# Optimization experiments

Hardware: AMD Instinct MI355X
Metric: run time of the kernel (lower is better)

## Reference

```python
import jax, jax.numpy as jnp
import numpy as np

L = 6        # flow_layers
DIM = 40     # state_dim = 4*levels
H = 128      # hidden_dim
ADIM = DIM // 2
DIN = ADIM + 2 * H  # x_a + ctx + t_e (cond_dim=0)
CLIP = 2.0   # flow_scale_clip
B = 131072


def _perm_mask_indices():
    # Matches ConditionalRealNVP.__init__(seed=0): per-layer permutation uses
    # default_rng(seed+i); masks drawn sequentially from default_rng(seed).
    rng = np.random.default_rng(0)
    perms, idx_a, idx_b = [], [], []
    for i in range(L):
        perms.append(np.random.default_rng(0 + i).permutation(DIM).astype(np.int32))
        mask = np.zeros(DIM, dtype=bool)
        mask[rng.choice(DIM, size=DIM // 2, replace=False)] = True
        idx_a.append(np.nonzero(mask)[0].astype(np.int32))
        idx_b.append(np.nonzero(~mask)[0].astype(np.int32))
    return (jnp.asarray(np.stack(perms)), jnp.asarray(np.stack(idx_a)),
            jnp.asarray(np.stack(idx_b)))


def setup_inputs() -> dict:
    key = jax.random.key(0)
    ks = jax.random.split(key, 16)

    def lin(k, shape, fan_in):
        bound = 1.0 / np.sqrt(fan_in)
        return jax.random.uniform(k, shape, jnp.float32, -bound, bound)

    x = jax.random.normal(ks[0], (B, DIM), jnp.float32)
    ctx = jax.random.normal(ks[1], (B, H), jnp.float32)
    t_e = jax.random.normal(ks[2], (B, H), jnp.float32)

    W1 = lin(ks[3], (L, DIN, H), DIN); b1 = lin(ks[4], (L, H), DIN)
    W2 = lin(ks[5], (L, H, H), H);     b2 = lin(ks[6], (L, H), H)
    W3 = lin(ks[7], (L, H, H), H);     b3 = lin(ks[8], (L, H), H)
    Ws = lin(ks[9], (L, H, ADIM), H);  bs = lin(ks[10], (L, ADIM), H)
    Wt = lin(ks[11], (L, H, ADIM), H); bt = lin(ks[12], (L, ADIM), H)

    perm, idx_a, idx_b = _perm_mask_indices()
    return dict(x=x, ctx=ctx, t_e=t_e, W1=W1, b1=b1, W2=W2, b2=b2, W3=W3, b3=b3,
                Ws=Ws, bs=bs, Wt=Wt, bt=bt, perm=perm, idx_a=idx_a, idx_b=idx_b)


def reference(x, ctx, t_e, W1, b1, W2, b2, W3, b3, Ws, bs, Wt, bt, perm, idx_a, idx_b):
    # ConditionalRealNVP.forward: per layer -> permute, mask-split, backbone MLP,
    # clamped affine scale/shift on x_b, scatter-merge, accumulate logdet.
    z = x
    logdet = jnp.zeros(x.shape[0], dtype=x.dtype)
    for i in range(L):
        z = z[:, perm[i]]                      # invertible permutation [B, DIM]
        z_a = z[:, idx_a[i]]                   # [B, ADIM] masked gather
        z_b = z[:, idx_b[i]]                   # [B, ADIM]
        h = jnp.concatenate([z_a, ctx, t_e], axis=-1)  # [B, DIN]
        h = jax.nn.silu(h @ W1[i] + b1[i])
        h = jax.nn.silu(h @ W2[i] + b2[i])
        h = jax.nn.silu(h @ W3[i] + b3[i])     # [B, H]
        s = jnp.clip(h @ Ws[i] + bs[i], -CLIP, CLIP)
        t = h @ Wt[i] + bt[i]
        y_b = z_b * jnp.exp(s) + t
        z = jnp.zeros_like(z).at[:, idx_a[i]].set(z_a).at[:, idx_b[i]].set(y_b)
        logdet = logdet + s.sum(axis=-1)
    return z, logdet
```

## Files before the change

kernel.cpp:

```cpp
#include <hip/hip_runtime.h>
#include <hip/hip_bf16.h>
#include <stdint.h>
#include <stddef.h>

typedef __bf16 bf16_t;
typedef __bf16 bf16x8 __attribute__((ext_vector_type(8)));
typedef __bf16 bf16x4 __attribute__((ext_vector_type(4)));
typedef float  f32x4  __attribute__((ext_vector_type(4)));

#define MFMA16(a, b, c) __builtin_amdgcn_mfma_f32_16x16x32_bf16((a), (b), (c), 0, 0, 0)

__device__ __forceinline__ float silu_f(float v) {
    return v * __builtin_amdgcn_rcpf(1.f + __expf(-v));
}

namespace cfg {
constexpr int B    = 131072;
constexpr int DIM  = 40;
constexpr int H    = 128;
constexpr int AD   = 20;
constexpr int L    = 6;
constexpr int MB   = 64;
constexpr int NTH  = 256;
constexpr int ZS   = 41;

constexpr int TILE  = 128 * 32;
constexpr int LTILE = 128 * 40;
constexpr int LSTR  = 21 * TILE;
constexpr int WTOT  = 6 * LSTR;
constexpr int NPH   = 6 * 21;

constexpr int CTE_BLKS = B / 16;
constexpr int W_BLKS   = WTOT / 256;
}

__device__ __align__(16) bf16_t g_wsb[cfg::WTOT];
__device__ int    g_gtab[352];
__device__ __align__(16) bf16_t g_cte[(size_t)cfg::B * 256];

__device__ __forceinline__ int woff(int an, int s) {
    return an * 40 + (((s ^ (an >> 1) ^ (an >> 3)) & 3) << 3);
}

__global__ void prep_all(const float* __restrict__ ctx, const float* __restrict__ te,
                         const float* __restrict__ W1, const float* __restrict__ W2,
                         const float* __restrict__ W3, const float* __restrict__ Ws,
                         const float* __restrict__ Wt, const int* __restrict__ perm,
                         const int* __restrict__ ia, const int* __restrict__ ib)
{
    using namespace cfg;
    __shared__ int phys_s[40], tmp_s[40], pas[20], pbs[20];
    __shared__ bf16_t cb[16 * 264];

    if (blockIdx.x < CTE_BLKS) {
        int g16 = blockIdx.x;
        int t = threadIdx.x;
        #pragma unroll
        for (int k = 0; k < 4; ++k) {
            int f4 = k * 256 + t;
            int r = f4 >> 6, c4 = (f4 & 63) * 4;
            const float* src = (c4 < 128) ? &ctx[((size_t)g16 * 16 + r) * 128 + c4]
                                          : &te[((size_t)g16 * 16 + r) * 128 + (c4 - 128)];
            float4 v = *(const float4*)src;
            bf16x4 bv;
            bv[0] = (bf16_t)v.x; bv[1] = (bf16_t)v.y; bv[2] = (bf16_t)v.z; bv[3] = (bf16_t)v.w;
            *(bf16x4*)&cb[r * 264 + c4] = bv;
        }
        __syncthreads();
        #pragma unroll
        for (int kk = 0; kk < 2; ++kk) {
            int t2 = kk * 256 + t;
            int kt = t2 >> 6, ln = t2 & 63, q = ln >> 4, c = ln & 15;
            bf16x8 o = *(const bf16x8*)&cb[c * 264 + kt * 32 + q * 8];
            *(bf16x8*)&g_cte[(size_t)g16 * 4096 + (size_t)t2 * 8] = o;
        }
        return;
    }

    int bb = blockIdx.x - CTE_BLKS;
    int t  = bb * 256 + threadIdx.x;
    {
        int i = t / LSTR, r = t % LSTR;
        int tile = r / TILE, r2 = r % TILE;
        int n = r2 >> 5, kl = r2 & 31;
        float v = 0.f;
        if (tile < 9) {
            int k = tile * 32 + kl;
            if (k < 20)       v = W1[(i * 276 + k) * 128 + n];
            else if (k >= 32) v = W1[(i * 276 + (k - 12)) * 128 + n];
        } else if (tile < 13) {
            int k = (tile - 9) * 32 + kl;
            v = W2[(i * 128 + k) * 128 + n];
        } else if (tile < 17) {
            int k = (tile - 13) * 32 + kl;
            v = W3[(i * 128 + k) * 128 + n];
        } else {
            int k = (tile - 17) * 32 + kl;
            if (n < 20)                 v = Ws[(i * 128 + k) * 20 + n];
            else if (n >= 32 && n < 52) v = Wt[(i * 128 + k) * 20 + (n - 32)];
        }
        g_wsb[t] = (bf16_t)v;
    }

    if (bb == 0) {
        int u = threadIdx.x;
        if (u < 40) phys_s[u] = u;
        __syncthreads();
        for (int i = 0; i < L; ++i) {
            if (u < 20) {
                int sa = phys_s[perm[i * 40 + ia[i * 20 + u]]];
                int sb = phys_s[perm[i * 40 + ib[i * 20 + u]]];
                pas[u] = sa; pbs[u] = sb;
                g_gtab[i * 32 + u]        = sa;
                g_gtab[192 + i * 20 + u]  = sb;
            } else if (u < 32) {
                g_gtab[i * 32 + u] = 0;
            }
            __syncthreads();
            if (u < 20) {
                tmp_s[ia[i * 20 + u]] = pas[u];
                tmp_s[ib[i * 20 + u]] = pbs[u];
            }
            __syncthreads();
            if (u < 40) phys_s[u] = tmp_s[u];
            __syncthreads();
        }
        if (u < 40) g_gtab[312 + u] = phys_s[u];
    }
}

__global__ __launch_bounds__(256, 3) void flow_main(
    const float* __restrict__ x,
    const float* __restrict__ gb1, const float* __restrict__ gb2, const float* __restrict__ gb3,
    const float* __restrict__ gbs, const float* __restrict__ gbt,
    float* __restrict__ out)
{
    using namespace cfg;
    __shared__ __align__(16) char smem[49792];
    float*  z_s  = (float*)(smem);
    bf16_t* h    = (bf16_t*)(smem + 10496);
    bf16_t* wb   = (bf16_t*)(smem + 27904);
    int*    gtab = (int*)(smem + 48384);

    const int tid  = threadIdx.x;
    const int lane = tid & 63;
    const int w    = tid >> 6;
    const int q    = lane >> 4, c = lane & 15;
    const int rw   = w * 16;
    const int cb   = w * 32 + 2 * c;
    const int row0 = blockIdx.x * MB;

    for (int e = tid; e < 352; e += NTH) gtab[e] = g_gtab[e];
    for (int e = tid; e < MB * DIM; e += NTH) {
        int r = e / DIM, d = e - r * DIM;
        z_s[r * ZS + d] = x[(size_t)row0 * DIM + e];
    }

    uint4 sg0, sg1;
    const int an0 = tid >> 2, sl0 = tid & 3;
    auto SLOAD = [&](int T) {
        const bf16_t* s = g_wsb + (size_t)T * TILE;
        sg0 = *(const uint4*)(s + tid * 8);
        sg1 = *(const uint4*)(s + 2048 + tid * 8);
    };
    auto SWRITE = [&](bf16_t* wbc) {
        *(uint4*)&wbc[woff(an0, sl0)]      = sg0;
        *(uint4*)&wbc[woff(an0 + 64, sl0)] = sg1;
    };

    SLOAD(0);
    SWRITE(wb);
    float ld[4] = {0.f, 0.f, 0.f, 0.f};
    __syncthreads();
    int cur = 0;

    for (int i = 0; i < L; ++i) {
        const int* pa = gtab + i * 32;
        const int* pb = gtab + 192 + i * 20;
        const int  T0 = i * 21;

        {
            f32x4 acc[4][2] = {};
            bf16x8 aN[4];
            #pragma unroll
            for (int kt = 0; kt < 9; ++kt) {
                bf16_t* wbc = wb + cur * LTILE;
                SLOAD(T0 + kt + 1);
                bf16x8 aK[4];
                if (kt == 0) {
                    #pragma unroll
                    for (int rf = 0; rf < 4; ++rf) {
                        bf16x8 t;
                        #pragma unroll
                        for (int j = 0; j < 8; ++j)
                            t[j] = (bf16_t)z_s[(rf * 16 + c) * ZS + pa[q * 8 + j]];
                        aK[rf] = t;
                    }
                    #pragma unroll
                    for (int rf = 0; rf < 4; ++rf)
                        aN[rf] = *(const bf16x8*)&g_cte[((size_t)(blockIdx.x * 4 + rf)) * 4096 + lane * 8];
                } else {
                    #pragma unroll
                    for (int rf = 0; rf < 4; ++rf) aK[rf] = aN[rf];
                    if (kt < 8) {
                        #pragma unroll
                        for (int rf = 0; rf < 4; ++rf)
                            aN[rf] = *(const bf16x8*)&g_cte[((size_t)(blockIdx.x * 4 + rf)) * 4096 + (size_t)kt * 512 + lane * 8];
                    }
                }
                bf16x8 b0 = *(const bf16x8*)&wbc[woff(cb, q)];
                bf16x8 b1 = *(const bf16x8*)&wbc[woff(cb + 1, q)];
                __builtin_amdgcn_s_setprio(1);
                #pragma unroll
                for (int rf = 0; rf < 4; ++rf) {
                    acc[rf][0] = MFMA16(aK[rf], b0, acc[rf][0]);
                    acc[rf][1] = MFMA16(aK[rf], b1, acc[rf][1]);
                }
                __builtin_amdgcn_s_setprio(0);
                if (kt == 8) {
                    float bv0 = gb1[i * H + cb], bv1 = gb1[i * H + cb + 1];
                    #pragma unroll
                    for (int rf = 0; rf < 4; ++rf)
                        #pragma unroll
                        for (int rr = 0; rr < 4; ++rr) {
                            float v0 = silu_f(acc[rf][0][rr] + bv0);
                            float v1 = silu_f(acc[rf][1][rr] + bv1);
                            union { bf16_t h2[2]; uint32_t u; } pk;
                            pk.h2[0] = (bf16_t)v0; pk.h2[1] = (bf16_t)v1;
                            *(uint32_t*)&h[(rf * 16 + q * 4 + rr) * 136 + cb] = pk.u;
                        }
                }
                SWRITE(wb + (cur ^ 1) * LTILE);
                __syncthreads();
                cur ^= 1;
            }
        }

        #pragma unroll
        for (int mm = 0; mm < 2; ++mm) {
            bf16x8 ah[16];
            #pragma unroll
            for (int kt = 0; kt < 4; ++kt)
                #pragma unroll
                for (int rf = 0; rf < 4; ++rf)
                    ah[kt * 4 + rf] = *(const bf16x8*)&h[(rf * 16 + c) * 136 + kt * 32 + q * 8];
            f32x4 acc[4][2] = {};
            const float* bias = (mm == 0 ? gb2 : gb3) + i * H;
            #pragma unroll
            for (int kt = 0; kt < 4; ++kt) {
                bf16_t* wbc = wb + cur * LTILE;
                SLOAD(T0 + 9 + mm * 4 + kt + 1);
                bf16x8 b0 = *(const bf16x8*)&wbc[woff(cb, q)];
                bf16x8 b1 = *(const bf16x8*)&wbc[woff(cb + 1, q)];
                __builtin_amdgcn_s_setprio(1);
                #pragma unroll
                for (int rf = 0; rf < 4; ++rf) {
                    acc[rf][0] = MFMA16(ah[kt * 4 + rf], b0, acc[rf][0]);
                    acc[rf][1] = MFMA16(ah[kt * 4 + rf], b1, acc[rf][1]);
                }
                __builtin_amdgcn_s_setprio(0);
                if (kt == 3) {
                    float bv0 = bias[cb], bv1 = bias[cb + 1];
                    #pragma unroll
                    for (int rf = 0; rf < 4; ++rf)
                        #pragma unroll
                        for (int rr = 0; rr < 4; ++rr) {
                            float v0 = silu_f(acc[rf][0][rr] + bv0);
                            float v1 = silu_f(acc[rf][1][rr] + bv1);
                            union { bf16_t h2[2]; uint32_t u; } pk;
                            pk.h2[0] = (bf16_t)v0; pk.h2[1] = (bf16_t)v1;
                            *(uint32_t*)&h[(rf * 16 + q * 4 + rr) * 136 + cb] = pk.u;
                        }
                }
                SWRITE(wb + (cur ^ 1) * LTILE);
                __syncthreads();
                cur ^= 1;
            }
        }

        {
            f32x4 sacc[4] = {};
            #pragma unroll
            for (int kt = 0; kt < 4; ++kt) {
                bf16_t* wbc = wb + cur * LTILE;
                int Tn = T0 + 18 + kt;
                if (Tn < NPH) SLOAD(Tn);
                bf16x8 af = *(const bf16x8*)&h[(rw + c) * 136 + kt * 32 + q * 8];
                __builtin_amdgcn_s_setprio(1);
                #pragma unroll
                for (int nt = 0; nt < 4; ++nt) {
                    bf16x8 bfr = *(const bf16x8*)&wbc[woff(nt * 16 + c, q)];
                    sacc[nt] = MFMA16(af, bfr, sacc[nt]);
                }
                __builtin_amdgcn_s_setprio(0);
                if (kt == 3) {
                    float bs0 = gbs[i * AD + c];
                    float bt0 = gbt[i * AD + c];
                    int   sl1 = pb[c];
                    float bs1 = 0.f, bt1 = 0.f; int sl2 = 0;
                    if (c < 4) { bs1 = gbs[i * AD + 16 + c]; bt1 = gbt[i * AD + 16 + c]; sl2 = pb[16 + c]; }
                    #pragma unroll
                    for (int rr = 0; rr < 4; ++rr) {
                        int row = rw + q * 4 + rr;
                        float s1 = fminf(fmaxf(sacc[0][rr] + bs0, -2.f), 2.f);
                        float y1 = z_s[row * ZS + sl1] * __expf(s1) + (sacc[2][rr] + bt0);
                        z_s[row * ZS + sl1] = y1;
                        float ssum = s1;
                        if (c < 4) {
                            float s2 = fminf(fmaxf(sacc[1][rr] + bs1, -2.f), 2.f);
                            float y2 = z_s[row * ZS + sl2] * __expf(s2) + (sacc[3][rr] + bt1);
                            z_s[row * ZS + sl2] = y2;
                            ssum += s2;
                        }
                        ssum += __shfl_xor(ssum, 1);
                        ssum += __shfl_xor(ssum, 2);
                        ssum += __shfl_xor(ssum, 4);
                        ssum += __shfl_xor(ssum, 8);
                        ld[rr] += ssum;
                    }
                }
                if (Tn < NPH) SWRITE(wb + (cur ^ 1) * LTILE);
                __syncthreads();
                cur ^= 1;
            }
        }
    }

    const int* fo = gtab + 312;
    for (int e = tid; e < MB * DIM; e += NTH) {
        int r = e / DIM, d = e - r * DIM;
        out[(size_t)row0 * DIM + e] = z_s[r * ZS + fo[d]];
    }
    if (c == 0) {
        #pragma unroll
        for (int rr = 0; rr < 4; ++rr)
            out[(size_t)B * DIM + row0 + rw + q * 4 + rr] = ld[rr];
    }
}

extern "C" void kernel_launch(void* const* d_in, const int* in_sizes, int n_in,
                              void* d_out, int out_size, void* d_ws, size_t ws_size,
                              hipStream_t stream) {
    using namespace cfg;
    const float* x   = (const float*)d_in[0];
    const float* ctx = (const float*)d_in[1];
    const float* te  = (const float*)d_in[2];
    const float* W1  = (const float*)d_in[3];
    const float* b1  = (const float*)d_in[4];
    const float* W2  = (const float*)d_in[5];
    const float* b2  = (const float*)d_in[6];
    const float* W3  = (const float*)d_in[7];
    const float* b3  = (const float*)d_in[8];
    const float* Ws_ = (const float*)d_in[9];
    const float* bs_ = (const float*)d_in[10];
    const float* Wt_ = (const float*)d_in[11];
    const float* bt_ = (const float*)d_in[12];
    const int* perm  = (const int*)d_in[13];
    const int* ia    = (const int*)d_in[14];
    const int* ib    = (const int*)d_in[15];

    float* out = (float*)d_out;

    prep_all<<<CTE_BLKS + W_BLKS, 256, 0, stream>>>(ctx, te, W1, W2, W3, Ws_, Wt_, perm, ia, ib);
    flow_main<<<B / MB, NTH, 0, stream>>>(x, b1, b2, b3, bs_, bt_, out);
}
```

Baseline: 482.7 us.

## Prefetch weight tiles two phases ahead with split-register staging and lighter barriers

Weight tile staging moves from one register set to two (A/B), so each global load is issued two phases before its LDS write rather than one, giving more time to hide global latency. The __syncthreads is replaced by a barrier that waits only on LDS/scalar counters (lgkmcnt), so outstanding global loads are not drained at each phase. The LDS weight row stride grows from 40 to 48 with a simpler XOR swizzle, which raises shared memory per block and adds staging registers, possibly hurting occupancy at 3 blocks/CU. The pipeline now restarts at each layer boundary, adding a prologue per layer.

```diff
diff --git a/kernel.cpp b/kernel.cpp
--- a/kernel.cpp
+++ b/kernel.cpp
@@ -13,6 +13,12 @@
 __device__ __forceinline__ float silu_f(float v) {
     return v * __builtin_amdgcn_rcpf(1.f + __expf(-v));
 }
+
+#define PHASE_BAR() do {                                   \
+    asm volatile("s_waitcnt lgkmcnt(0)" ::: "memory");     \
+    __builtin_amdgcn_s_barrier();                          \
+    __builtin_amdgcn_sched_barrier(0);                     \
+} while (0)
 
 namespace cfg {
 constexpr int B    = 131072;
@@ -25,10 +31,9 @@
 constexpr int ZS   = 41;
 
 constexpr int TILE  = 128 * 32;
-constexpr int LTILE = 128 * 40;
+constexpr int LTILE = 128 * 48;
 constexpr int LSTR  = 21 * TILE;
 constexpr int WTOT  = 6 * LSTR;
-constexpr int NPH   = 6 * 21;
 
 constexpr int CTE_BLKS = B / 16;
 constexpr int W_BLKS   = WTOT / 256;
@@ -39,7 +44,7 @@
 __device__ __align__(16) bf16_t g_cte[(size_t)cfg::B * 256];
 
 __device__ __forceinline__ int woff(int an, int s) {
-    return an * 40 + (((s ^ (an >> 1) ^ (an >> 3)) & 3) << 3);
+    return an * 48 + ((s ^ ((an >> 1) & 3)) << 3);
 }
 
 __global__ void prep_all(const float* __restrict__ ctx, const float* __restrict__ te,
@@ -136,11 +141,11 @@
     float* __restrict__ out)
 {
     using namespace cfg;
-    __shared__ __align__(16) char smem[49792];
+    __shared__ __align__(16) char smem[53888];
     float*  z_s  = (float*)(smem);
     bf16_t* h    = (bf16_t*)(smem + 10496);
     bf16_t* wb   = (bf16_t*)(smem + 27904);
-    int*    gtab = (int*)(smem + 48384);
+    int*    gtab = (int*)(smem + 52480);
 
     const int tid  = threadIdx.x;
     const int lane = tid & 63;
@@ -156,38 +161,42 @@
         z_s[r * ZS + d] = x[(size_t)row0 * DIM + e];
     }
 
-    uint4 sg0, sg1;
+    uint4 sgA0, sgA1, sgB0, sgB1;
     const int an0 = tid >> 2, sl0 = tid & 3;
-    auto SLOAD = [&](int T) {
-        const bf16_t* s = g_wsb + (size_t)T * TILE;
-        sg0 = *(const uint4*)(s + tid * 8);
-        sg1 = *(const uint4*)(s + 2048 + tid * 8);
-    };
-    auto SWRITE = [&](bf16_t* wbc) {
-        *(uint4*)&wbc[woff(an0, sl0)]      = sg0;
-        *(uint4*)&wbc[woff(an0 + 64, sl0)] = sg1;
-    };
-
-    SLOAD(0);
-    SWRITE(wb);
+#define SLOADP(P, T) do { const bf16_t* _s = g_wsb + (size_t)(T) * cfg::TILE;              \
+        if ((P) == 0) { sgA0 = *(const uint4*)(_s + (size_t)tid * 8);                      \
+                        sgA1 = *(const uint4*)(_s + 2048 + (size_t)tid * 8); }             \
+        else          { sgB0 = *(const uint4*)(_s + (size_t)tid * 8);                      \
+                        sgB1 = *(const uint4*)(_s + 2048 + (size_t)tid * 8); } } while (0)
+#define SWRITEP(P, wbc) do {                                                               \
+        if ((P) == 0) { *(uint4*)&(wbc)[woff(an0, sl0)]      = sgA0;                       \
+                        *(uint4*)&(wbc)[woff(an0 + 64, sl0)] = sgA1; }                     \
+        else          { *(uint4*)&(wbc)[woff(an0, sl0)]      = sgB0;                       \
+                        *(uint4*)&(wbc)[woff(an0 + 64, sl0)] = sgB1; } } while (0)
+
     float ld[4] = {0.f, 0.f, 0.f, 0.f};
     __syncthreads();
-    int cur = 0;
 
     for (int i = 0; i < L; ++i) {
         const int* pa = gtab + i * 32;
         const int* pb = gtab + 192 + i * 20;
         const int  T0 = i * 21;
 
+        SLOADP(0, T0);
+        SWRITEP(0, wb);
+        SLOADP(1, T0 + 1);
+        PHASE_BAR();
+
         {
             f32x4 acc[4][2] = {};
             bf16x8 aN[4];
             #pragma unroll
-            for (int kt = 0; kt < 9; ++kt) {
-                bf16_t* wbc = wb + cur * LTILE;
-                SLOAD(T0 + kt + 1);
+            for (int pl = 0; pl < 9; ++pl) {
+                const int S = pl & 1;
+                bf16_t* wbc = wb + S * LTILE;
+                SLOADP(S, T0 + pl + 2);
                 bf16x8 aK[4];
-                if (kt == 0) {
+                if (pl == 0) {
                     #pragma unroll
                     for (int rf = 0; rf < 4; ++rf) {
                         bf16x8 t;
@@ -202,10 +211,10 @@
                 } else {
                     #pragma unroll
                     for (int rf = 0; rf < 4; ++rf) aK[rf] = aN[rf];
-                    if (kt < 8) {
+                    if (pl < 8) {
                         #pragma unroll
                         for (int rf = 0; rf < 4; ++rf)
-                            aN[rf] = *(const bf16x8*)&g_cte[((size_t)(blockIdx.x * 4 + rf)) * 4096 + (size_t)kt * 512 + lane * 8];
+                            aN[rf] = *(const bf16x8*)&g_cte[((size_t)(blockIdx.x * 4 + rf)) * 4096 + (size_t)pl * 512 + lane * 8];
                     }
                 }
                 bf16x8 b0 = *(const bf16x8*)&wbc[woff(cb, q)];
@@ -217,7 +226,7 @@
                     acc[rf][1] = MFMA16(aK[rf], b1, acc[rf][1]);
                 }
                 __builtin_amdgcn_s_setprio(0);
-                if (kt == 8) {
+                if (pl == 8) {
                     float bv0 = gb1[i * H + cb], bv1 = gb1[i * H + cb + 1];
                     #pragma unroll
                     for (int rf = 0; rf < 4; ++rf)
@@ -230,9 +239,8 @@
                             *(uint32_t*)&h[(rf * 16 + q * 4 + rr) * 136 + cb] = pk.u;
                         }
                 }
-                SWRITE(wb + (cur ^ 1) * LTILE);
-                __syncthreads();
-                cur ^= 1;
+                SWRITEP(S ^ 1, wb + (S ^ 1) * LTILE);
+                PHASE_BAR();
             }
         }
 
@@ -248,8 +256,10 @@
             const float* bias = (mm == 0 ? gb2 : gb3) + i * H;
             #pragma unroll
             for (int kt = 0; kt < 4; ++kt) {
-                bf16_t* wbc = wb + cur * LTILE;
-                SLOAD(T0 + 9 + mm * 4 + kt + 1);
+                const int pl = 9 + mm * 4 + kt;
+                const int S = pl & 1;
+                bf16_t* wbc = wb + S * LTILE;
+                SLOADP(S, T0 + pl + 2);
                 bf16x8 b0 = *(const bf16x8*)&wbc[woff(cb, q)];
                 bf16x8 b1 = *(const bf16x8*)&wbc[woff(cb + 1, q)];
                 __builtin_amdgcn_s_setprio(1);
@@ -272,9 +282,8 @@
                             *(uint32_t*)&h[(rf * 16 + q * 4 + rr) * 136 + cb] = pk.u;
                         }
                 }
-                SWRITE(wb + (cur ^ 1) * LTILE);
-                __syncthreads();
-                cur ^= 1;
+                SWRITEP(S ^ 1, wb + (S ^ 1) * LTILE);
+                PHASE_BAR();
             }
         }
 
@@ -282,9 +291,10 @@
             f32x4 sacc[4] = {};
             #pragma unroll
             for (int kt = 0; kt < 4; ++kt) {
-                bf16_t* wbc = wb + cur * LTILE;
-                int Tn = T0 + 18 + kt;
-                if (Tn < NPH) SLOAD(Tn);
+                const int pl = 17 + kt;
+                const int S = pl & 1;
+                bf16_t* wbc = wb + S * LTILE;
+                if (pl <= 18) SLOADP(S, T0 + pl + 2);
                 bf16x8 af = *(const bf16x8*)&h[(rw + c) * 136 + kt * 32 + q * 8];
                 __builtin_amdgcn_s_setprio(1);
                 #pragma unroll
@@ -319,9 +329,8 @@
                         ld[rr] += ssum;
                     }
                 }
-                if (Tn < NPH) SWRITE(wb + (cur ^ 1) * LTILE);
-                __syncthreads();
-                cur ^= 1;
+                if (pl <= 19) SWRITEP(S ^ 1, wb + (S ^ 1) * LTILE);
+                PHASE_BAR();
             }
         }
     }
@@ -336,6 +345,8 @@
         for (int rr = 0; rr < 4; ++rr)
             out[(size_t)B * DIM + row0 + rw + q * 4 + rr] = ld[rr];
     }
+#undef SLOADP
+#undef SWRITEP
 }
 
 extern "C" void kernel_launch(void* const* d_in, const int* in_sizes, int n_in,
```

Result: slower. 507.3 us (+5.1%).
